# Kernel tuning notes

Hardware: AMD Instinct MI355X
Metric: run time of the kernel (lower is better)

## Reference

```python
import jax, jax.numpy as jnp
import numpy as np

B, D, DEPTH, C = 8192, 2048, 10, 1000
NUM_INNER = 2 ** DEPTH - 1   # 1023
NUM_LEAVES = 2 ** DEPTH      # 1024


def setup_inputs() -> dict:
    key = jax.random.key(0)
    k1, k2, k3, k4 = jax.random.split(key, 4)
    x = jax.random.normal(k1, (B, D), dtype=jnp.float32)
    # scale weights like a typical init so sigmoid isn't fully saturated
    W = jax.random.normal(k2, (D, NUM_INNER), dtype=jnp.float32) * 0.02
    b = jax.random.normal(k3, (NUM_INNER,), dtype=jnp.float32) * 0.02
    leaf_dist = jax.random.normal(k4, (NUM_LEAVES, C), dtype=jnp.float32)
    return {"x": x, "W": W, "b": b, "leaf_dist": leaf_dist}


def reference(x, W, b, leaf_dist):
    # inner node routing probabilities: [B, num_inner]
    decisions = jax.nn.sigmoid(x @ W + b)
    depth = int(np.log2(decisions.shape[1] + 1))
    pp = jnp.ones((x.shape[0], 1), dtype=x.dtype)  # path probs, starts at root
    for d in range(depth):  # small fixed loop over tree depth
        s, e = 2 ** d - 1, 2 ** (d + 1) - 1
        ld = decisions[:, s:e]                      # [B, 2^d]
        pp = jnp.concatenate([pp * ld, pp * (1.0 - ld)], axis=1)  # [B, 2^(d+1)]
        # faithful reproduction of the original's even/odd reordering
        pp = jnp.concatenate([pp[:, ::2], pp[:, 1::2]], axis=1)
    leaf_probs = jax.nn.softmax(leaf_dist, axis=1)  # [num_leaves, C]
    return pp @ leaf_probs                          # [B, C]
```

## Files before the change

kernel.cpp:

```cpp
#include <hip/hip_runtime.h>

typedef __attribute__((ext_vector_type(8))) unsigned short ushort8v;
typedef __attribute__((ext_vector_type(8))) __bf16 bf16x8;
typedef __attribute__((ext_vector_type(4))) float floatx4;

__device__ __forceinline__ unsigned short f2b(float f) {
    unsigned u = __float_as_uint(f);
    unsigned r = u + 0x7fffu + ((u >> 16) & 1u);
    return (unsigned short)(r >> 16);
}
__device__ __forceinline__ float b2f(unsigned short h) {
    return __uint_as_float(((unsigned)h) << 16);
}

__device__ __forceinline__ void async_cp16(const void* g, void* l) {
    __builtin_amdgcn_global_load_lds(
        (__attribute__((address_space(1))) void*)g,
        (__attribute__((address_space(3))) void*)l,
        16, 0, 0);
}

__global__ __launch_bounds__(256) void prep_kernel(const float* __restrict__ x,
                                                   unsigned short* __restrict__ xb,
                                                   const float* __restrict__ W,
                                                   unsigned short* __restrict__ Wt,
                                                   const float* __restrict__ ld_,
                                                   unsigned short* __restrict__ P) {
    __shared__ float tile[32 * 33];
    __shared__ float buf[1000];
    __shared__ float red[8];
    const int b = blockIdx.x, t = threadIdx.x;
    if (b < 16384) {
        int i = b * 256 + t;
        float4 v = ((const float4*)x)[i];
        ushort4 o;
        o.x = f2b(v.x); o.y = f2b(v.y); o.z = f2b(v.z); o.w = f2b(v.w);
        ((ushort4*)xb)[i] = o;
    } else if (b < 16384 + 2048) {
        int idx = b - 16384;
        int n0 = (idx & 31) * 32, k0 = (idx >> 5) * 32;
        int tx = t & 31, ty = t >> 5;
#pragma unroll
        for (int i = 0; i < 4; i++) {
            int k = k0 + ty + i * 8, n = n0 + tx;
            tile[(ty + i * 8) * 33 + tx] = (n < 1023) ? W[(size_t)k * 1023 + n] : 0.f;
        }
        __syncthreads();
#pragma unroll
        for (int i = 0; i < 4; i++) {
            int n = n0 + ty + i * 8, k = k0 + tx;
            Wt[(size_t)n * 2048 + k] = f2b(tile[tx * 33 + ty + i * 8]);
        }
    } else {
        int row = b - 18432;
        const float* r = ld_ + (size_t)row * 1000;
        float mx = -3.4e38f;
        for (int i = t; i < 1000; i += 256) { float v = r[i]; buf[i] = v; mx = fmaxf(mx, v); }
#pragma unroll
        for (int o = 32; o > 0; o >>= 1) mx = fmaxf(mx, __shfl_down(mx, o));
        if ((t & 63) == 0) red[t >> 6] = mx;
        __syncthreads();
        mx = fmaxf(fmaxf(red[0], red[1]), fmaxf(red[2], red[3]));
        float s = 0.f;
        for (int i = t; i < 1000; i += 256) { float e = __expf(buf[i] - mx); buf[i] = e; s += e; }
#pragma unroll
        for (int o = 32; o > 0; o >>= 1) s += __shfl_down(s, o);
        if ((t & 63) == 0) red[4 + (t >> 6)] = s;
        __syncthreads();
        float inv = 1.f / (red[4] + red[5] + red[6] + red[7]);
        unsigned short* out = P + (size_t)row * 1000;
        for (int i = t; i < 1000; i += 256) out[i] = f2b(buf[i] * inv);
    }
}

__global__ __launch_bounds__(256) void pp_transP_kernel(unsigned short* __restrict__ dec,
                                                        const unsigned short* __restrict__ P,
                                                        unsigned short* __restrict__ Pt) {
    __shared__ float smem[3072];
    const int b = blockIdx.x, t = threadIdx.x;
    if (b < 8192) {
        float* d = smem; float* pa = smem + 1024; float* pb = smem + 2048;
        unsigned short* row = dec + (size_t)b * 1024;
        for (int i = t; i < 1024; i += 256) d[i] = (i < 1023) ? b2f(row[i]) : 0.f;
        if (t == 0) pa[0] = 1.f;
        __syncthreads();
        float* cur = pa; float* nxt = pb;
        for (int dep = 0; dep < 10; dep++) {
            const int half = 1 << dep;
            const int len = half << 1;
            for (int j = t; j < len; j += 256) {
                int tt = j >> dep;
                int s  = j & (half - 1);
                int i2 = 2 * s + tt;
                int u  = i2 >> dep;
                int rr = i2 & (half - 1);
                float dv = d[half - 1 + rr];
                nxt[j] = cur[rr] * (u ? (1.f - dv) : dv);
            }
            __syncthreads();
            float* tmp = cur; cur = nxt; nxt = tmp;
        }
        for (int i = t; i < 1024; i += 256) row[i] = f2b(cur[i]);
    } else {
        int idx = b - 8192;
        int c0 = (idx & 31) * 32, l0 = (idx >> 5) * 32;
        int tx = t & 31, ty = t >> 5;
        unsigned short* tile = (unsigned short*)smem;
#pragma unroll
        for (int i = 0; i < 4; i++) {
            int c = c0 + tx, l = l0 + ty + i * 8;
            tile[(ty + i * 8) * 33 + tx] = (c < 1000) ? P[(size_t)l * 1000 + c] : (unsigned short)0;
        }
        __syncthreads();
#pragma unroll
        for (int i = 0; i < 4; i++) {
            Pt[(size_t)(c0 + ty + i * 8) * 1024 + l0 + tx] = tile[tx * 33 + ty + i * 8];
        }
    }
}

#define BM 64
#define BN 128
#define BK 32

template <int EPI>
__global__ __launch_bounds__(256, 4) void gemm_bt(const unsigned short* __restrict__ A,
                                                  const unsigned short* __restrict__ Bt,
                                                  const float* __restrict__ bias,
                                                  unsigned short* __restrict__ obf,
                                                  float* __restrict__ of32,
                                                  int K, int ldo) {
    __shared__ __align__(16) unsigned short As[BM * BK];
    __shared__ __align__(16) unsigned short Bs[BN * BK];
    const int tid  = threadIdx.x;
    const int lane = tid & 63;
    const int wave = tid >> 6;
    const int wrow = (wave >> 1) * 32;
    const int wcol = (wave & 1) * 64;
    const int quad = lane >> 4, l16 = lane & 15;

    const int l   = blockIdx.x;
    const int xcd = l & 7;
    const int j   = l >> 3;
    const int bm  = (xcd * 16 + (j & 15)) * BM;
    const int bn  = (j >> 4) * BN;

    const int srow = tid >> 2;
    const int lg   = (tid & 3) ^ ((srow >> 1) & 3);
    const int scol = lg * 8;

    const unsigned short* Ag = A + (size_t)(bm + srow) * K + scol;
    const unsigned short* Bg = Bt + (size_t)(bn + srow) * K + scol;
    unsigned short* AsW = As + wave * 512;
    unsigned short* BsW = Bs + wave * 512;

    const int pg = (quad ^ ((l16 >> 1) & 3)) * 8;

    floatx4 acc[2][4] = {};

    for (int k0 = 0; k0 < K; k0 += BK) {
        async_cp16(Ag + k0, AsW);
        async_cp16(Bg + k0, BsW);
        async_cp16(Bg + (size_t)64 * K + k0, BsW + 2048);
        __syncthreads();

        bf16x8 af[2], bfr[4];
#pragma unroll
        for (int mi = 0; mi < 2; mi++)
            af[mi] = __builtin_bit_cast(bf16x8,
                *(const ushort8v*)(As + (wrow + mi * 16 + l16) * BK + pg));
#pragma unroll
        for (int ni = 0; ni < 4; ni++)
            bfr[ni] = __builtin_bit_cast(bf16x8,
                *(const ushort8v*)(Bs + (wcol + ni * 16 + l16) * BK + pg));
#pragma unroll
        for (int mi = 0; mi < 2; mi++)
#pragma unroll
            for (int ni = 0; ni < 4; ni++)
                acc[mi][ni] = __builtin_amdgcn_mfma_f32_16x16x32_bf16(
                    af[mi], bfr[ni], acc[mi][ni], 0, 0, 0);
        __syncthreads();
    }

#pragma unroll
    for (int ni = 0; ni < 4; ni++) {
        const int col = bn + wcol + ni * 16 + l16;
        float bb = 0.f;
        if constexpr (EPI == 0) bb = (col < 1023) ? bias[col] : 0.f;
#pragma unroll
        for (int mi = 0; mi < 2; mi++) {
            const int row0 = bm + wrow + mi * 16 + quad * 4;
#pragma unroll
            for (int r = 0; r < 4; r++) {
                float v = acc[mi][ni][r];
                if constexpr (EPI == 0) {
                    float sgm = 1.f / (1.f + __expf(-(v + bb)));
                    obf[(size_t)(row0 + r) * ldo + col] = f2b(sgm);
                } else {
                    if (col < 1000) of32[(size_t)(row0 + r) * ldo + col] = v;
                }
            }
        }
    }
}

extern "C" void kernel_launch(void* const* d_in, const int* in_sizes, int n_in,
                              void* d_out, int out_size, void* d_ws, size_t ws_size,
                              hipStream_t stream) {
    const float* x   = (const float*)d_in[0];
    const float* W   = (const float*)d_in[1];
    const float* b   = (const float*)d_in[2];
    const float* ldd = (const float*)d_in[3];
    float* out = (float*)d_out;

    char* ws = (char*)d_ws;
    unsigned short* xb  = (unsigned short*)(ws);
    unsigned short* Wt  = (unsigned short*)(ws + 33554432);
    unsigned short* dec = (unsigned short*)(ws + 37748736);
    unsigned short* P   = (unsigned short*)(ws + 54525952);
    unsigned short* Pt  = (unsigned short*)(ws + 56574208);

    prep_kernel<<<16384 + 2048 + 1024, 256, 0, stream>>>(x, xb, W, Wt, ldd, P);
    gemm_bt<0><<<1024, 256, 0, stream>>>(xb, Wt, b, dec, nullptr, 2048, 1024);
    pp_transP_kernel<<<8192 + 1024, 256, 0, stream>>>(dec, P, Pt);
    gemm_bt<1><<<1024, 256, 0, stream>>>(dec, Pt, nullptr, nullptr, out, 1024, 1000);
}
```

Before: 219.4 us.

## Double-buffer LDS tiles with BK=64 to overlap global loads with MFMA

The bf16 GEMM main loop now uses two LDS buffers and a K-tile of 64, so the async global-to-LDS copies for the next tile are issued before the MFMAs on the current tile. This hides load latency and halves the number of barriers per K. The LDS swizzle is redone for 64-wide rows. The larger shared-memory footprint lowers the occupancy hint from 4 to 3 blocks per CU. Only one barrier per iteration guards both buffers, which relies on the async-copy completion semantics holding at that barrier.

```diff
diff --git a/kernel.cpp b/kernel.cpp
--- a/kernel.cpp
+++ b/kernel.cpp
@@ -121,17 +121,17 @@
 
 #define BM 64
 #define BN 128
-#define BK 32
+#define BK 64
 
 template <int EPI>
-__global__ __launch_bounds__(256, 4) void gemm_bt(const unsigned short* __restrict__ A,
+__global__ __launch_bounds__(256, 3) void gemm_bt(const unsigned short* __restrict__ A,
                                                   const unsigned short* __restrict__ Bt,
                                                   const float* __restrict__ bias,
                                                   unsigned short* __restrict__ obf,
                                                   float* __restrict__ of32,
                                                   int K, int ldo) {
-    __shared__ __align__(16) unsigned short As[BM * BK];
-    __shared__ __align__(16) unsigned short Bs[BN * BK];
+    __shared__ __align__(16) unsigned short As[2][BM * BK];
+    __shared__ __align__(16) unsigned short Bs[2][BN * BK];
     const int tid  = threadIdx.x;
     const int lane = tid & 63;
     const int wave = tid >> 6;
@@ -145,40 +145,71 @@
     const int bm  = (xcd * 16 + (j & 15)) * BM;
     const int bn  = (j >> 4) * BN;
 
-    const int srow = tid >> 2;
-    const int lg   = (tid & 3) ^ ((srow >> 1) & 3);
-    const int scol = lg * 8;
-
-    const unsigned short* Ag = A + (size_t)(bm + srow) * K + scol;
-    const unsigned short* Bg = Bt + (size_t)(bn + srow) * K + scol;
-    unsigned short* AsW = As + wave * 512;
-    unsigned short* BsW = Bs + wave * 512;
-
-    const int pg = (quad ^ ((l16 >> 1) & 3)) * 8;
+    const int lr = lane >> 3;
+    const int lc = lane & 7;
+    const int ce = (lc ^ lr) * 8;
+    size_t aoff[2], boff[4];
+#pragma unroll
+    for (int ja = 0; ja < 2; ja++)
+        aoff[ja] = (size_t)(bm + 16 * wave + 8 * ja + lr) * K + ce;
+#pragma unroll
+    for (int jb = 0; jb < 4; jb++)
+        boff[jb] = (size_t)(bn + 32 * wave + 8 * jb + lr) * K + ce;
+
+    const int rA  = l16 & 7;
+    const int ka0 = (quad ^ rA) * 8;
+    const int ka1 = ((quad + 4) ^ rA) * 8;
 
     floatx4 acc[2][4] = {};
 
-    for (int k0 = 0; k0 < K; k0 += BK) {
-        async_cp16(Ag + k0, AsW);
-        async_cp16(Bg + k0, BsW);
-        async_cp16(Bg + (size_t)64 * K + k0, BsW + 2048);
-        __syncthreads();
-
-        bf16x8 af[2], bfr[4];
-#pragma unroll
-        for (int mi = 0; mi < 2; mi++)
-            af[mi] = __builtin_bit_cast(bf16x8,
-                *(const ushort8v*)(As + (wrow + mi * 16 + l16) * BK + pg));
-#pragma unroll
-        for (int ni = 0; ni < 4; ni++)
-            bfr[ni] = __builtin_bit_cast(bf16x8,
-                *(const ushort8v*)(Bs + (wcol + ni * 16 + l16) * BK + pg));
-#pragma unroll
-        for (int mi = 0; mi < 2; mi++)
-#pragma unroll
-            for (int ni = 0; ni < 4; ni++)
-                acc[mi][ni] = __builtin_amdgcn_mfma_f32_16x16x32_bf16(
-                    af[mi], bfr[ni], acc[mi][ni], 0, 0, 0);
+    {
+        char* ab = (char*)As[0];
+        char* bb = (char*)Bs[0];
+#pragma unroll
+        for (int ja = 0; ja < 2; ja++) async_cp16(A + aoff[ja], ab + (2 * wave + ja) * 1024);
+#pragma unroll
+        for (int jb = 0; jb < 4; jb++) async_cp16(Bt + boff[jb], bb + (4 * wave + jb) * 1024);
+    }
+    __syncthreads();
+
+    const int NIT = K >> 6;
+    for (int it = 0; it < NIT; it++) {
+        const int cur = it & 1;
+        if (it + 1 < NIT) {
+            const int k0 = (it + 1) << 6;
+            char* ab = (char*)As[cur ^ 1];
+            char* bb = (char*)Bs[cur ^ 1];
+#pragma unroll
+            for (int ja = 0; ja < 2; ja++)
+                async_cp16(A + aoff[ja] + k0, ab + (2 * wave + ja) * 1024);
+#pragma unroll
+            for (int jb = 0; jb < 4; jb++)
+                async_cp16(Bt + boff[jb] + k0, bb + (4 * wave + jb) * 1024);
+        }
+
+        const unsigned short* as = As[cur];
+        const unsigned short* bs = Bs[cur];
+        bf16x8 af[2][2], bfr[2][4];
+#pragma unroll
+        for (int mi = 0; mi < 2; mi++) {
+            const unsigned short* rp = as + (wrow + mi * 16 + l16) * BK;
+            af[0][mi] = __builtin_bit_cast(bf16x8, *(const ushort8v*)(rp + ka0));
+            af[1][mi] = __builtin_bit_cast(bf16x8, *(const ushort8v*)(rp + ka1));
+        }
+#pragma unroll
+        for (int ni = 0; ni < 4; ni++) {
+            const unsigned short* rp = bs + (wcol + ni * 16 + l16) * BK;
+            bfr[0][ni] = __builtin_bit_cast(bf16x8, *(const ushort8v*)(rp + ka0));
+            bfr[1][ni] = __builtin_bit_cast(bf16x8, *(const ushort8v*)(rp + ka1));
+        }
+#pragma unroll
+        for (int kk = 0; kk < 2; kk++)
+#pragma unroll
+            for (int mi = 0; mi < 2; mi++)
+#pragma unroll
+                for (int ni = 0; ni < 4; ni++)
+                    acc[mi][ni] = __builtin_amdgcn_mfma_f32_16x16x32_bf16(
+                        af[kk][mi], bfr[kk][ni], acc[mi][ni], 0, 0, 0);
         __syncthreads();
     }
 
```

After: 225.4 us. 2.7% more time.

## Pre-pack GEMM operands into MFMA fragment layout and drop LDS staging

Applied to the files above, without the earlier changes.

The prep and path-probability kernels now write x, W, the leaf softmax and the path probabilities directly in a per-16-row fragment-blocked bf16 layout matching the MFMA operand order. The GEMMs then load fragments straight from global memory into registers with no LDS staging or barriers. The separate transpose of P is folded into the softmax blocks. This removes shared-memory traffic and synchronisation, but each wave now reads its operands from global memory with no reuse across waves through LDS, which leans on L2 and raises global load traffic.

```diff
diff --git a/kernel.cpp b/kernel.cpp
--- a/kernel.cpp
+++ b/kernel.cpp
@@ -13,33 +13,36 @@
     return __uint_as_float(((unsigned)h) << 16);
 }
 
-__device__ __forceinline__ void async_cp16(const void* g, void* l) {
-    __builtin_amdgcn_global_load_lds(
-        (__attribute__((address_space(1))) void*)g,
-        (__attribute__((address_space(3))) void*)l,
-        16, 0, 0);
-}
 
 __global__ __launch_bounds__(256) void prep_kernel(const float* __restrict__ x,
-                                                   unsigned short* __restrict__ xb,
+                                                   unsigned short* __restrict__ A2x,
                                                    const float* __restrict__ W,
-                                                   unsigned short* __restrict__ Wt,
+                                                   unsigned short* __restrict__ B2w,
                                                    const float* __restrict__ ld_,
-                                                   unsigned short* __restrict__ P) {
+                                                   unsigned short* __restrict__ B2p) {
     __shared__ float tile[32 * 33];
     __shared__ float buf[1000];
     __shared__ float red[8];
     const int b = blockIdx.x, t = threadIdx.x;
-    if (b < 16384) {
-        int i = b * 256 + t;
-        float4 v = ((const float4*)x)[i];
-        ushort4 o;
-        o.x = f2b(v.x); o.y = f2b(v.y); o.z = f2b(v.z); o.w = f2b(v.w);
-        ((ushort4*)xb)[i] = o;
-    } else if (b < 16384 + 2048) {
-        int idx = b - 16384;
-        int n0 = (idx & 31) * 32, k0 = (idx >> 5) * 32;
-        int tx = t & 31, ty = t >> 5;
+    if (b < 512) {
+        const int mt = b;
+        const int wave = t >> 6, kco = (t >> 4) & 3, l16 = t & 15;
+        const float* xr0 = x + (size_t)(mt * 16 + l16) * 2048;
+#pragma unroll 4
+        for (int i = 0; i < 16; i++) {
+            const int kc = wave * 64 + i * 4 + kco;
+            const float* xr = xr0 + kc * 8;
+            float4 v0 = *(const float4*)xr;
+            float4 v1 = *(const float4*)(xr + 4);
+            ushort8v o;
+            o[0] = f2b(v0.x); o[1] = f2b(v0.y); o[2] = f2b(v0.z); o[3] = f2b(v0.w);
+            o[4] = f2b(v1.x); o[5] = f2b(v1.y); o[6] = f2b(v1.z); o[7] = f2b(v1.w);
+            *(ushort8v*)(A2x + ((size_t)(mt * 256 + kc) * 16 + l16) * 8) = o;
+        }
+    } else if (b < 2560) {
+        const int idx = b - 512;
+        const int n0 = (idx & 31) * 32, k0 = (idx >> 5) * 32;
+        const int tx = t & 31, ty = t >> 5;
 #pragma unroll
         for (int i = 0; i < 4; i++) {
             int k = k0 + ty + i * 8, n = n0 + tx;
@@ -49,11 +52,12 @@
 #pragma unroll
         for (int i = 0; i < 4; i++) {
             int n = n0 + ty + i * 8, k = k0 + tx;
-            Wt[(size_t)n * 2048 + k] = f2b(tile[tx * 33 + ty + i * 8]);
+            size_t off = ((size_t)((n >> 4) * 256 + (k >> 3)) * 16 + (n & 15)) * 8 + (k & 7);
+            B2w[off] = f2b(tile[tx * 33 + ty + i * 8]);
         }
     } else {
-        int row = b - 18432;
-        const float* r = ld_ + (size_t)row * 1000;
+        const int l0 = b - 2560;
+        const float* r = ld_ + (size_t)l0 * 1000;
         float mx = -3.4e38f;
         for (int i = t; i < 1000; i += 256) { float v = r[i]; buf[i] = v; mx = fmaxf(mx, v); }
 #pragma unroll
@@ -68,128 +72,108 @@
         if ((t & 63) == 0) red[4 + (t >> 6)] = s;
         __syncthreads();
         float inv = 1.f / (red[4] + red[5] + red[6] + red[7]);
-        unsigned short* out = P + (size_t)row * 1000;
-        for (int i = t; i < 1000; i += 256) out[i] = f2b(buf[i] * inv);
-    }
-}
-
-__global__ __launch_bounds__(256) void pp_transP_kernel(unsigned short* __restrict__ dec,
-                                                        const unsigned short* __restrict__ P,
-                                                        unsigned short* __restrict__ Pt) {
-    __shared__ float smem[3072];
-    const int b = blockIdx.x, t = threadIdx.x;
-    if (b < 8192) {
-        float* d = smem; float* pa = smem + 1024; float* pb = smem + 2048;
-        unsigned short* row = dec + (size_t)b * 1024;
-        for (int i = t; i < 1024; i += 256) d[i] = (i < 1023) ? b2f(row[i]) : 0.f;
-        if (t == 0) pa[0] = 1.f;
-        __syncthreads();
-        float* cur = pa; float* nxt = pb;
-        for (int dep = 0; dep < 10; dep++) {
-            const int half = 1 << dep;
-            const int len = half << 1;
-            for (int j = t; j < len; j += 256) {
-                int tt = j >> dep;
-                int s  = j & (half - 1);
-                int i2 = 2 * s + tt;
-                int u  = i2 >> dep;
-                int rr = i2 & (half - 1);
-                float dv = d[half - 1 + rr];
-                nxt[j] = cur[rr] * (u ? (1.f - dv) : dv);
-            }
-            __syncthreads();
-            float* tmp = cur; cur = nxt; nxt = tmp;
-        }
-        for (int i = t; i < 1024; i += 256) row[i] = f2b(cur[i]);
-    } else {
-        int idx = b - 8192;
-        int c0 = (idx & 31) * 32, l0 = (idx >> 5) * 32;
-        int tx = t & 31, ty = t >> 5;
-        unsigned short* tile = (unsigned short*)smem;
-#pragma unroll
-        for (int i = 0; i < 4; i++) {
-            int c = c0 + tx, l = l0 + ty + i * 8;
-            tile[(ty + i * 8) * 33 + tx] = (c < 1000) ? P[(size_t)l * 1000 + c] : (unsigned short)0;
-        }
-        __syncthreads();
-#pragma unroll
-        for (int i = 0; i < 4; i++) {
-            Pt[(size_t)(c0 + ty + i * 8) * 1024 + l0 + tx] = tile[tx * 33 + ty + i * 8];
-        }
-    }
-}
-
-#define BM 64
-#define BN 128
-#define BK 32
+        for (int i = t; i < 1024; i += 256) {
+            float pv = (i < 1000) ? buf[i] * inv : 0.f;
+            size_t off = ((size_t)((i >> 4) * 128 + (l0 >> 3)) * 16 + (i & 15)) * 8 + (l0 & 7);
+            B2p[off] = f2b(pv);
+        }
+    }
+}
+
+__global__ __launch_bounds__(256) void pp_kernel(const unsigned short* __restrict__ dec,
+                                                 unsigned short* __restrict__ A2p) {
+    __shared__ float d[1024];
+    __shared__ float pa[1024], pb[1024];
+    const int t = threadIdx.x;
+    const int rrow = blockIdx.x;
+    const unsigned short* row = dec + (size_t)rrow * 1024;
+    for (int i = t; i < 1024; i += 256) d[i] = (i < 1023) ? b2f(row[i]) : 0.f;
+    if (t == 0) pa[0] = 1.f;
+    __syncthreads();
+    float* cur = pa; float* nxt = pb;
+    for (int dep = 0; dep < 10; dep++) {
+        const int half = 1 << dep;
+        const int len = half << 1;
+        for (int j = t; j < len; j += 256) {
+            int tt = j >> dep;
+            int s  = j & (half - 1);
+            int i2 = 2 * s + tt;
+            int u  = i2 >> dep;
+            int rr = i2 & (half - 1);
+            float dv = d[half - 1 + rr];
+            nxt[j] = cur[rr] * (u ? (1.f - dv) : dv);
+        }
+        __syncthreads();
+        float* tmp = cur; cur = nxt; nxt = tmp;
+    }
+    const int mtb = (rrow >> 4) * 128;
+    const int li  = (rrow & 15) * 8;
+    for (int i = t; i < 1024; i += 256) {
+        size_t off = ((size_t)(mtb + (i >> 3)) * 16) * 8 + li + (i & 7);
+        A2p[off] = f2b(cur[i]);
+    }
+}
 
 template <int EPI>
-__global__ __launch_bounds__(256, 4) void gemm_bt(const unsigned short* __restrict__ A,
-                                                  const unsigned short* __restrict__ Bt,
-                                                  const float* __restrict__ bias,
-                                                  unsigned short* __restrict__ obf,
-                                                  float* __restrict__ of32,
-                                                  int K, int ldo) {
-    __shared__ __align__(16) unsigned short As[BM * BK];
-    __shared__ __align__(16) unsigned short Bs[BN * BK];
+__global__ __launch_bounds__(256, 4) void gemm_frag(const unsigned short* __restrict__ A2,
+                                                    const unsigned short* __restrict__ B2,
+                                                    const float* __restrict__ bias,
+                                                    unsigned short* __restrict__ obf,
+                                                    float* __restrict__ of32,
+                                                    int KC, int ldo) {
     const int tid  = threadIdx.x;
     const int lane = tid & 63;
     const int wave = tid >> 6;
-    const int wrow = (wave >> 1) * 32;
-    const int wcol = (wave & 1) * 64;
+    const int wr = wave >> 1, wc = wave & 1;
     const int quad = lane >> 4, l16 = lane & 15;
 
     const int l   = blockIdx.x;
     const int xcd = l & 7;
     const int j   = l >> 3;
-    const int bm  = (xcd * 16 + (j & 15)) * BM;
-    const int bn  = (j >> 4) * BN;
-
-    const int srow = tid >> 2;
-    const int lg   = (tid & 3) ^ ((srow >> 1) & 3);
-    const int scol = lg * 8;
-
-    const unsigned short* Ag = A + (size_t)(bm + srow) * K + scol;
-    const unsigned short* Bg = Bt + (size_t)(bn + srow) * K + scol;
-    unsigned short* AsW = As + wave * 512;
-    unsigned short* BsW = Bs + wave * 512;
-
-    const int pg = (quad ^ ((l16 >> 1) & 3)) * 8;
+    const int bmt = xcd * 16 + (j & 15);
+    const int bnt = j >> 4;
+
+    const int mt0 = bmt * 4 + wr * 2;
+    const int nt0 = bnt * 8 + wc * 4;
+
+    const int lofs = (quad * 16 + l16) * 8;
+    const unsigned short* a0 = A2 + (size_t)(mt0 + 0) * KC * 128 + lofs;
+    const unsigned short* a1 = A2 + (size_t)(mt0 + 1) * KC * 128 + lofs;
+    const unsigned short* b0 = B2 + (size_t)(nt0 + 0) * KC * 128 + lofs;
+    const unsigned short* b1 = B2 + (size_t)(nt0 + 1) * KC * 128 + lofs;
+    const unsigned short* b2 = B2 + (size_t)(nt0 + 2) * KC * 128 + lofs;
+    const unsigned short* b3 = B2 + (size_t)(nt0 + 3) * KC * 128 + lofs;
 
     floatx4 acc[2][4] = {};
-
-    for (int k0 = 0; k0 < K; k0 += BK) {
-        async_cp16(Ag + k0, AsW);
-        async_cp16(Bg + k0, BsW);
-        async_cp16(Bg + (size_t)64 * K + k0, BsW + 2048);
-        __syncthreads();
-
-        bf16x8 af[2], bfr[4];
-#pragma unroll
-        for (int mi = 0; mi < 2; mi++)
-            af[mi] = __builtin_bit_cast(bf16x8,
-                *(const ushort8v*)(As + (wrow + mi * 16 + l16) * BK + pg));
-#pragma unroll
-        for (int ni = 0; ni < 4; ni++)
-            bfr[ni] = __builtin_bit_cast(bf16x8,
-                *(const ushort8v*)(Bs + (wcol + ni * 16 + l16) * BK + pg));
-#pragma unroll
-        for (int mi = 0; mi < 2; mi++)
-#pragma unroll
-            for (int ni = 0; ni < 4; ni++)
-                acc[mi][ni] = __builtin_amdgcn_mfma_f32_16x16x32_bf16(
-                    af[mi], bfr[ni], acc[mi][ni], 0, 0, 0);
-        __syncthreads();
+    const int NIT = KC >> 2;
+
+#pragma unroll 2
+    for (int it = 0; it < NIT; it++) {
+        const size_t ko = (size_t)it * 512;
+        bf16x8 af0 = __builtin_bit_cast(bf16x8, *(const ushort8v*)(a0 + ko));
+        bf16x8 af1 = __builtin_bit_cast(bf16x8, *(const ushort8v*)(a1 + ko));
+        bf16x8 bf0 = __builtin_bit_cast(bf16x8, *(const ushort8v*)(b0 + ko));
+        bf16x8 bf1 = __builtin_bit_cast(bf16x8, *(const ushort8v*)(b1 + ko));
+        bf16x8 bf2 = __builtin_bit_cast(bf16x8, *(const ushort8v*)(b2 + ko));
+        bf16x8 bf3 = __builtin_bit_cast(bf16x8, *(const ushort8v*)(b3 + ko));
+        acc[0][0] = __builtin_amdgcn_mfma_f32_16x16x32_bf16(af0, bf0, acc[0][0], 0, 0, 0);
+        acc[0][1] = __builtin_amdgcn_mfma_f32_16x16x32_bf16(af0, bf1, acc[0][1], 0, 0, 0);
+        acc[0][2] = __builtin_amdgcn_mfma_f32_16x16x32_bf16(af0, bf2, acc[0][2], 0, 0, 0);
+        acc[0][3] = __builtin_amdgcn_mfma_f32_16x16x32_bf16(af0, bf3, acc[0][3], 0, 0, 0);
+        acc[1][0] = __builtin_amdgcn_mfma_f32_16x16x32_bf16(af1, bf0, acc[1][0], 0, 0, 0);
+        acc[1][1] = __builtin_amdgcn_mfma_f32_16x16x32_bf16(af1, bf1, acc[1][1], 0, 0, 0);
+        acc[1][2] = __builtin_amdgcn_mfma_f32_16x16x32_bf16(af1, bf2, acc[1][2], 0, 0, 0);
+        acc[1][3] = __builtin_amdgcn_mfma_f32_16x16x32_bf16(af1, bf3, acc[1][3], 0, 0, 0);
     }
 
 #pragma unroll
     for (int ni = 0; ni < 4; ni++) {
-        const int col = bn + wcol + ni * 16 + l16;
+        const int col = (nt0 + ni) * 16 + l16;
         float bb = 0.f;
         if constexpr (EPI == 0) bb = (col < 1023) ? bias[col] : 0.f;
 #pragma unroll
         for (int mi = 0; mi < 2; mi++) {
-            const int row0 = bm + wrow + mi * 16 + quad * 4;
+            const int row0 = (mt0 + mi) * 16 + quad * 4;
 #pragma unroll
             for (int r = 0; r < 4; r++) {
                 float v = acc[mi][ni][r];
@@ -214,14 +198,14 @@
     float* out = (float*)d_out;
 
     char* ws = (char*)d_ws;
-    unsigned short* xb  = (unsigned short*)(ws);
-    unsigned short* Wt  = (unsigned short*)(ws + 33554432);
+    unsigned short* A2x = (unsigned short*)(ws);
+    unsigned short* A2p = (unsigned short*)(ws);
+    unsigned short* B2w = (unsigned short*)(ws + 33554432);
     unsigned short* dec = (unsigned short*)(ws + 37748736);
-    unsigned short* P   = (unsigned short*)(ws + 54525952);
-    unsigned short* Pt  = (unsigned short*)(ws + 56574208);
-
-    prep_kernel<<<16384 + 2048 + 1024, 256, 0, stream>>>(x, xb, W, Wt, ldd, P);
-    gemm_bt<0><<<1024, 256, 0, stream>>>(xb, Wt, b, dec, nullptr, 2048, 1024);
-    pp_transP_kernel<<<8192 + 1024, 256, 0, stream>>>(dec, P, Pt);
-    gemm_bt<1><<<1024, 256, 0, stream>>>(dec, Pt, nullptr, nullptr, out, 1024, 1000);
-}
+    unsigned short* B2p = (unsigned short*)(ws + 54525952);
+
+    prep_kernel<<<3584, 256, 0, stream>>>(x, A2x, W, B2w, ldd, B2p);
+    gemm_frag<0><<<1024, 256, 0, stream>>>(A2x, B2w, b, dec, nullptr, 256, 1024);
+    pp_kernel<<<8192, 256, 0, stream>>>(dec, A2p);
+    gemm_frag<1><<<1024, 256, 0, stream>>>(A2p, B2p, nullptr, nullptr, out, 128, 1000);
+}
```

Result: slower. 226.1 us (+3.0%).
